# Kernel optimization log

Hardware: AMD Instinct MI355X
Metric: run time of the kernel (lower is better)

Reference implementation:

```python
import jax, jax.numpy as jnp
import numpy as np

B, T, D = 2, 2048, 1024
H = 16
HD = D // H
SCALE = 1.0 / np.sqrt(HD).astype(np.float32)


def setup_inputs() -> dict:
    key = jax.random.key(0)
    ks = jax.random.split(key, 5)
    std = 1.0 / np.sqrt(D).astype(np.float32)
    x = jax.random.normal(ks[0], (B, T, D), dtype=jnp.float32)
    Wqkvt = jax.random.normal(ks[1], (D, 4 * D), dtype=jnp.float32) * std
    bqkvt = jax.random.normal(ks[2], (4 * D,), dtype=jnp.float32) * 0.02
    Wout = jax.random.normal(ks[3], (D, D), dtype=jnp.float32) * std
    bout = jax.random.normal(ks[4], (D,), dtype=jnp.float32) * 0.02
    return {"x": x, "Wqkvt": Wqkvt, "bqkvt": bqkvt, "Wout": Wout, "bout": bout}


def reference(x, Wqkvt, bqkvt, Wout, bout):
    b, t, d = x.shape
    # fused qkvt projection -> [B,T,4,H,HD]
    qkvt = (x @ Wqkvt + bqkvt).reshape(b, t, 4, H, HD)
    # -> [B,H,T,HD] each
    q, k, v, tt = [jnp.transpose(qkvt[:, :, i], (0, 2, 1, 3)) for i in range(4)]

    # standard dot-product scores [B,H,T,T]
    scores_dot = jnp.einsum('bhqd,bhkd->bhqk', q, k)
    # triplet term: (q*t) against cumsum over keys of (k*v)/sqrt(hd)
    kv = k * v * SCALE
    kv_cum = jnp.cumsum(kv, axis=2)  # causal prefix over key positions
    scores_trip = jnp.einsum('bhqd,bhkd->bhqk', q * tt, kv_cum)

    scores = (scores_dot + scores_trip) * SCALE
    causal = jnp.triu(jnp.ones((t, t), dtype=bool), k=1)
    scores = jnp.where(causal[None, None], -jnp.inf, scores)

    attn = jax.nn.softmax(scores, axis=-1)
    out = jnp.einsum('bhqk,bhkd->bhqd', attn, v)  # [B,H,T,HD]
    out = jnp.transpose(out, (0, 2, 1, 3)).reshape(b, t, d)
    return out @ Wout + bout
```

## Files before the change

kernel.cpp:

```cpp
#include <hip/hip_runtime.h>

#define T_SEQ 2048
#define D_MODEL 1024
#define NH 16
#define HD 64
#define BH_TOT 32
#define M_ROWS 4096
#define NT 32
#define SCALE 0.125f
#define BHT (BH_TOT * T_SEQ)
#define LOG2E 1.44269504f
#define TAU 2.885f

typedef _Float16 h8 __attribute__((ext_vector_type(8)));
typedef _Float16 h4 __attribute__((ext_vector_type(4)));
typedef float f32x4 __attribute__((ext_vector_type(4)));

__device__ __forceinline__ f32x4 mfma_h(h8 a, h8 b, f32x4 c) {
    return __builtin_amdgcn_mfma_f32_16x16x32_f16(a, b, c, 0, 0, 0);
}

__device__ __forceinline__ void gload16(const _Float16* g, _Float16* l) {
    __builtin_amdgcn_global_load_lds(
        (const __attribute__((address_space(1))) unsigned int*)g,
        (__attribute__((address_space(3))) unsigned int*)l, 16, 0, 0);
}

__global__ void k_convert(const float* __restrict__ in, _Float16* __restrict__ out, int n) {
    int i = (blockIdx.x * blockDim.x + threadIdx.x) * 4;
    if (i < n) {
        float4 v = *(const float4*)(in + i);
        h4 o;
        o[0] = (_Float16)v.x; o[1] = (_Float16)v.y;
        o[2] = (_Float16)v.z; o[3] = (_Float16)v.w;
        *(h4*)(out + i) = o;
    }
}

__global__ void k_transpose(const float* __restrict__ in, _Float16* __restrict__ out, int K, int N) {
    __shared__ float tile[32][33];
    int nb = blockIdx.x * 32, kb = blockIdx.y * 32;
    int tx = threadIdx.x & 31, ty = threadIdx.x >> 5;
    #pragma unroll
    for (int i = 0; i < 32; i += 8)
        tile[ty + i][tx] = in[(size_t)(kb + ty + i) * N + (nb + tx)];
    __syncthreads();
    #pragma unroll
    for (int i = 0; i < 32; i += 8)
        out[(size_t)(nb + ty + i) * K + (kb + tx)] = (_Float16)tile[tx][ty + i];
}

template<int MODE>
__launch_bounds__(256, 2)
__global__ void k_gemm(const _Float16* __restrict__ A, const _Float16* __restrict__ Bt,
                       int M, int N, int K, const float* __restrict__ bias,
                       _Float16* __restrict__ qo, _Float16* __restrict__ kho,
                       _Float16* __restrict__ kfo, _Float16* __restrict__ vo,
                       _Float16* __restrict__ vfo, _Float16* __restrict__ to,
                       float* __restrict__ cOut)
{
    __shared__ __align__(16) _Float16 lA[2][128 * 64];
    __shared__ __align__(16) _Float16 lB[2][128 * 64];
    const int tid = threadIdx.x;
    const int wid = tid >> 6, lane = tid & 63, lrow = lane & 15, lg = lane >> 4;
    const int wm = wid >> 1, wn = wid & 1;
    const int m0 = blockIdx.x * 128, n0 = blockIdx.y * 128;

    f32x4 acc[4][4];
    #pragma unroll
    for (int i = 0; i < 4; i++)
        #pragma unroll
        for (int j = 0; j < 4; j++) acc[i][j] = (f32x4){0.f, 0.f, 0.f, 0.f};

    const int rin = lane >> 3, gcol = lane & 7;
    const int scol = (gcol ^ rin) * 8;
    const _Float16* gA = A + (size_t)(m0 + 32 * wid + rin) * K + scol;
    const _Float16* gB = Bt + (size_t)(n0 + 32 * wid + rin) * K + scol;

    const int r7 = lrow & 7;
    const int nk = K >> 6;

    #pragma unroll
    for (int i = 0; i < 4; i++) {
        gload16(gA + (size_t)(8 * i) * K, &lA[0][32 * wid * 64 + 8 * i * 64]);
        gload16(gB + (size_t)(8 * i) * K, &lB[0][32 * wid * 64 + 8 * i * 64]);
    }
    __syncthreads();

    for (int kt = 0; kt < nk; ++kt) {
        const int cur = kt & 1;
        if (kt + 1 < nk) {
            const size_t ko = (size_t)(kt + 1) * 64;
            #pragma unroll
            for (int i = 0; i < 4; i++) {
                gload16(gA + (size_t)(8 * i) * K + ko, &lA[cur ^ 1][32 * wid * 64 + 8 * i * 64]);
                gload16(gB + (size_t)(8 * i) * K + ko, &lB[cur ^ 1][32 * wid * 64 + 8 * i * 64]);
            }
        }
        h8 af[4][2], bfr[4][2];
        #pragma unroll
        for (int mi = 0; mi < 4; mi++) {
            const int row = wm * 64 + mi * 16 + lrow;
            af[mi][0] = *(const h8*)&lA[cur][row * 64 + ((lg ^ r7) * 8)];
            af[mi][1] = *(const h8*)&lA[cur][row * 64 + (((4 + lg) ^ r7) * 8)];
        }
        #pragma unroll
        for (int ni = 0; ni < 4; ni++) {
            const int row = wn * 64 + ni * 16 + lrow;
            bfr[ni][0] = *(const h8*)&lB[cur][row * 64 + ((lg ^ r7) * 8)];
            bfr[ni][1] = *(const h8*)&lB[cur][row * 64 + (((4 + lg) ^ r7) * 8)];
        }
        #pragma unroll
        for (int mi = 0; mi < 4; mi++)
            #pragma unroll
            for (int ni = 0; ni < 4; ni++) {
                acc[mi][ni] = mfma_h(af[mi][0], bfr[ni][0], acc[mi][ni]);
                acc[mi][ni] = mfma_h(af[mi][1], bfr[ni][1], acc[mi][ni]);
            }
        __syncthreads();
    }

    if (MODE == 0) {
        const int ssel = n0 >> 10;
        #pragma unroll
        for (int mi = 0; mi < 4; mi++) {
            #pragma unroll
            for (int ni = 0; ni < 4; ni++) {
                const int nn = n0 + wn * 64 + ni * 16 + lrow;
                const float bv = bias[nn];
                const int h = (nn >> 6) & 15, hd = nn & 63;
                const int mmb = m0 + wm * 64 + mi * 16 + 4 * lg;
                const int b = mmb >> 11, t0 = mmb & (T_SEQ - 1);
                const int bh = b * NH + h;
                const size_t rowb = (size_t)bh * T_SEQ;
                h4 hv;
                #pragma unroll
                for (int r = 0; r < 4; r++) hv[r] = (_Float16)(acc[mi][ni][r] + bv);
                if (ssel == 0) {
                    #pragma unroll
                    for (int r = 0; r < 4; r++) qo[(rowb + t0 + r) * HD + hd] = hv[r];
                } else if (ssel == 1) {
                    const int ksK = hd >> 5, lgK = (hd & 31) >> 3, iK = hd & 7;
                    #pragma unroll
                    for (int r = 0; r < 4; r++) {
                        const int t = t0 + r;
                        kho[(rowb + t) * HD + hd] = hv[r];
                        const int j = t >> 6, ct = (t >> 4) & 3;
                        const int laneF = (t & 15) | (lgK << 4);
                        kfo[(((size_t)bh * 32 + j) * 16 + ct * 4 + ksK) * 512 + laneF * 8 + iK] = hv[r];
                    }
                } else if (ssel == 2) {
                    #pragma unroll
                    for (int r = 0; r < 4; r++) vo[(rowb + t0 + r) * HD + hd] = hv[r];
                    const int ctV = hd >> 4, lrV = hd & 15;
                    const int j = t0 >> 6, ksV = (t0 >> 5) & 1, lgV = (t0 >> 3) & 3, i0 = t0 & 7;
                    const int laneF = lrV | (lgV << 4);
                    *(h4*)&vfo[(((size_t)bh * 32 + j) * 8 + ctV * 2 + ksV) * 512 + laneF * 8 + i0] = hv;
                } else {
                    #pragma unroll
                    for (int r = 0; r < 4; r++) to[(rowb + t0 + r) * HD + hd] = hv[r];
                }
            }
        }
    } else {
        #pragma unroll
        for (int mi = 0; mi < 4; mi++) {
            #pragma unroll
            for (int ni = 0; ni < 4; ni++) {
                const int nn = n0 + wn * 64 + ni * 16 + lrow;
                const float bv = bias[nn];
                #pragma unroll
                for (int r = 0; r < 4; r++) {
                    const int mm = m0 + wm * 64 + mi * 16 + 4 * lg + r;
                    cOut[(size_t)mm * N + nn] = acc[mi][ni][r] + bv;
                }
            }
        }
    }
}

__global__ void k_kvcum(const _Float16* __restrict__ Kh, const _Float16* __restrict__ Vh,
                        _Float16* __restrict__ KF)
{
    const int bh = blockIdx.x;
    const int w = threadIdx.x >> 6, d = threadIdx.x & 63;
    const size_t base = (size_t)bh * T_SEQ * HD + d;
    const int CH = T_SEQ / 16;
    const int t0 = w * CH;
    float s = 0.f;
    #pragma unroll 8
    for (int i = 0; i < CH; i++) {
        size_t o = base + (size_t)(t0 + i) * HD;
        s += (float)Kh[o] * (float)Vh[o];
    }
    __shared__ float tot[16][64];
    tot[w][d] = s;
    __syncthreads();
    float acc = 0.f;
    for (int ww = 0; ww < w; ww++) acc += tot[ww][d];
    const int ksK = 2 + (d >> 5), lgK = (d & 31) >> 3, iK = d & 7;
    for (int i = 0; i < CH; i++) {
        const int t = t0 + i;
        size_t o = base + (size_t)t * HD;
        acc += (float)Kh[o] * (float)Vh[o];
        const int j = t >> 6, ct = (t >> 4) & 3;
        const int laneF = (t & 15) | (lgK << 4);
        KF[(((size_t)bh * 32 + j) * 16 + ct * 4 + ksK) * 512 + laneF * 8 + iK] =
            (_Float16)(acc * SCALE);
    }
}

__launch_bounds__(256, 4)
__global__ void k_attn(const _Float16* __restrict__ Qb, const _Float16* __restrict__ Tb,
                       const _Float16* __restrict__ KF, const _Float16* __restrict__ VF,
                       _Float16* __restrict__ Op0, _Float16* __restrict__ Op1,
                       _Float16* __restrict__ Op2, _Float16* __restrict__ Op3,
                       float* __restrict__ ML, int nsplit)
{
    const int bh = blockIdx.x;
    const int pair = blockIdx.y;
    const int ksel = blockIdx.z;
    const int tid = threadIdx.x;
    const int wid = tid >> 6, lane = tid & 63, lrow = lane & 15, lg = lane >> 4;
    const _Float16* qp = Qb + (size_t)bh * T_SEQ * HD;
    const _Float16* tp = Tb + (size_t)bh * T_SEQ * HD;
    const _Float16* kfb = KF + (size_t)bh * 32 * 16 * 512;
    const _Float16* vfb = VF + (size_t)bh * 32 * 8 * 512;
    _Float16* op = (ksel == 0) ? Op0 : (ksel == 1) ? Op1 : (ksel == 2) ? Op2 : Op3;
    float* ml = ML + (size_t)ksel * BHT * 2;

    __shared__ __align__(16) _Float16 lP[4][16 * 64];

    const h8 ones = {(_Float16)1.f, (_Float16)1.f, (_Float16)1.f, (_Float16)1.f,
                     (_Float16)1.f, (_Float16)1.f, (_Float16)1.f, (_Float16)1.f};
    const float C = SCALE * LOG2E;

    for (int half = 0; half < 2; ++half) {
        const int qi = half ? (NT - 1 - pair) : pair;
        const int q0 = qi * 64;
        const int nj = qi + 1;
        const int jbeg = (nj * ksel) / nsplit;
        const int jend = (nj * (ksel + 1)) / nsplit;

        const int qrow = q0 + wid * 16 + lrow;
        h8 qf[4];
        #pragma unroll
        for (int ks = 0; ks < 2; ++ks) {
            h8 qv = *(const h8*)&qp[(size_t)qrow * HD + ks * 32 + lg * 8];
            h8 tv = *(const h8*)&tp[(size_t)qrow * HD + ks * 32 + lg * 8];
            h8 a2, b2;
            #pragma unroll
            for (int i = 0; i < 8; i++) {
                float qq = (float)qv[i] * C;
                a2[i] = (_Float16)qq;
                b2[i] = (_Float16)(qq * (float)tv[i]);
            }
            qf[ks] = a2; qf[2 + ks] = b2;
        }

        float m_r[4];
        f32x4 o[4], o4;
        #pragma unroll
        for (int r = 0; r < 4; r++) m_r[r] = -__builtin_inff();
        #pragma unroll
        for (int ct = 0; ct < 4; ct++) o[ct] = (f32x4){0.f, 0.f, 0.f, 0.f};
        o4 = (f32x4){0.f, 0.f, 0.f, 0.f};

        for (int j = jbeg; j < jend; ++j) {
            f32x4 s[4];
            #pragma unroll
            for (int ct = 0; ct < 4; ct++) {
                const _Float16* kb = kfb + ((size_t)j * 16 + ct * 4) * 512 + lane * 8;
                f32x4 sv = (f32x4){0.f, 0.f, 0.f, 0.f};
                sv = mfma_h(qf[0], *(const h8*)kb, sv);
                sv = mfma_h(qf[1], *(const h8*)(kb + 512), sv);
                sv = mfma_h(qf[2], *(const h8*)(kb + 1024), sv);
                sv = mfma_h(qf[3], *(const h8*)(kb + 1536), sv);
                s[ct] = sv;
            }
            if (j == qi) {
                #pragma unroll
                for (int ct = 0; ct < 4; ct++)
                    #pragma unroll
                    for (int r = 0; r < 4; r++) {
                        int key = j * 64 + ct * 16 + lrow;
                        int qr  = q0 + wid * 16 + 4 * lg + r;
                        if (key > qr) s[ct][r] = -__builtin_inff();
                    }
            }
            float mx[4];
            #pragma unroll
            for (int r = 0; r < 4; r++)
                mx[r] = fmaxf(fmaxf(s[0][r], s[1][r]), fmaxf(s[2][r], s[3][r]));
            bool need = (mx[0] > m_r[0] + TAU) | (mx[1] > m_r[1] + TAU) |
                        (mx[2] > m_r[2] + TAU) | (mx[3] > m_r[3] + TAU);
            if (__any(need)) {
                #pragma unroll
                for (int d = 1; d < 16; d <<= 1)
                    #pragma unroll
                    for (int r = 0; r < 4; r++) mx[r] = fmaxf(mx[r], __shfl_xor(mx[r], d, 64));
                #pragma unroll
                for (int r = 0; r < 4; r++) {
                    float mn = fmaxf(m_r[r], mx[r]);
                    float scl = __builtin_amdgcn_exp2f(m_r[r] - mn);
                    o[0][r] *= scl; o[1][r] *= scl; o[2][r] *= scl; o[3][r] *= scl;
                    o4[r] *= scl;
                    m_r[r] = mn;
                }
            }
            #pragma unroll
            for (int ct = 0; ct < 4; ct++) {
                const int col = ct * 16 + lrow;
                #pragma unroll
                for (int r = 0; r < 4; r++) {
                    float p = __builtin_amdgcn_exp2f(s[ct][r] - m_r[r]);
                    const int row = 4 * lg + r;
                    const int boff = row * 128 + ((col * 2) ^ ((row & 7) << 4) ^ ((row & 12) << 3));
                    lP[wid][boff >> 1] = (_Float16)p;
                }
            }
            h8 pa[2];
            #pragma unroll
            for (int ks = 0; ks < 2; ks++) {
                const int boff = lrow * 128 +
                    ((ks * 64 + lg * 16) ^ ((lrow & 7) << 4) ^ ((lrow & 12) << 3));
                pa[ks] = *(const h8*)((const char*)lP[wid] + boff);
            }
            o4 = mfma_h(pa[0], ones, o4);
            o4 = mfma_h(pa[1], ones, o4);
            #pragma unroll
            for (int ct = 0; ct < 4; ct++) {
                const _Float16* vb = vfb + ((size_t)j * 8 + ct * 2) * 512 + lane * 8;
                o[ct] = mfma_h(pa[0], *(const h8*)vb, o[ct]);
                o[ct] = mfma_h(pa[1], *(const h8*)(vb + 512), o[ct]);
            }
        }
        #pragma unroll
        for (int ct = 0; ct < 4; ct++)
            #pragma unroll
            for (int r = 0; r < 4; r++) {
                const int trow = q0 + wid * 16 + 4 * lg + r;
                const int d = ct * 16 + lrow;
                op[((size_t)bh * T_SEQ + trow) * HD + d] = (_Float16)o[ct][r];
            }
        if (lrow == 0) {
            #pragma unroll
            for (int r = 0; r < 4; r++) {
                const int trow = q0 + wid * 16 + 4 * lg + r;
                const size_t mi = ((size_t)bh * T_SEQ + trow) * 2;
                ml[mi] = m_r[r];
                ml[mi + 1] = o4[r];
            }
        }
    }
}

__global__ void k_combine(const _Float16* __restrict__ Op0, const _Float16* __restrict__ Op1,
                          const _Float16* __restrict__ Op2, const _Float16* __restrict__ Op3,
                          const float* __restrict__ ML, _Float16* __restrict__ AO, int nsplit)
{
    const int idx = blockIdx.x * 256 + threadIdx.x;
    const int row = idx >> 3;
    const int d0 = (idx & 7) * 8;
    const int bh = row >> 11, t = row & (T_SEQ - 1);
    const int b = bh >> 4, h = bh & 15;
    const _Float16* ops[4] = {Op0, Op1, Op2, Op3};
    float m = -__builtin_inff();
    for (int c = 0; c < nsplit; c++) m = fmaxf(m, ML[(size_t)c * BHT * 2 + 2 * row]);
    float w[4], denom = 0.f;
    for (int c = 0; c < nsplit; c++) {
        w[c] = __builtin_amdgcn_exp2f(ML[(size_t)c * BHT * 2 + 2 * row] - m);
        denom += w[c] * ML[(size_t)c * BHT * 2 + 2 * row + 1];
    }
    const float inv = 1.0f / denom;
    float accv[8];
    #pragma unroll
    for (int i = 0; i < 8; i++) accv[i] = 0.f;
    for (int c = 0; c < nsplit; c++) {
        h8 a = *(const h8*)&ops[c][(size_t)row * HD + d0];
        #pragma unroll
        for (int i = 0; i < 8; i++) accv[i] += w[c] * (float)a[i];
    }
    h8 r;
    #pragma unroll
    for (int i = 0; i < 8; i++) r[i] = (_Float16)(accv[i] * inv);
    *(h8*)&AO[((size_t)(b * T_SEQ + t)) * D_MODEL + h * HD + d0] = r;
}

extern "C" void kernel_launch(void* const* d_in, const int* in_sizes, int n_in,
                              void* d_out, int out_size, void* d_ws, size_t ws_size,
                              hipStream_t stream)
{
    const float* x     = (const float*)d_in[0];
    const float* Wqkvt = (const float*)d_in[1];
    const float* bqkvt = (const float*)d_in[2];
    const float* Wout  = (const float*)d_in[3];
    const float* bout  = (const float*)d_in[4];
    float* out = (float*)d_out;

    char* ws = (char*)d_ws;
    size_t off = 0;
    auto alloc = [&](size_t bytes) {
        char* p = ws + off;
        off += (bytes + 255) & ~(size_t)255;
        return p;
    };
    const size_t SZ = (size_t)M_ROWS * D_MODEL * 2;
    _Float16* xb  = (_Float16*)alloc(SZ);
    _Float16* wt  = (_Float16*)alloc(SZ);
    _Float16* wo  = (_Float16*)alloc((size_t)D_MODEL * D_MODEL * 2);
    _Float16* Qh  = (_Float16*)alloc(SZ);
    _Float16* Kh  = (_Float16*)alloc(SZ);
    _Float16* Vh  = (_Float16*)alloc(SZ);
    _Float16* Th  = (_Float16*)alloc(SZ);
    _Float16* KF  = (_Float16*)alloc(SZ * 2);
    _Float16* VF  = (_Float16*)alloc(SZ);
    _Float16* AO  = (_Float16*)alloc(SZ);
    _Float16* Op3 = (_Float16*)alloc(SZ);
    const size_t need4 = off;

    const int nsplit = (ws_size >= need4) ? 4 : 2;

    _Float16* Op0 = xb;
    _Float16* Op1 = Vh;
    _Float16* Op2 = Kh;
    float*    ML  = (float*)wt;

    k_convert<<<4096, 256, 0, stream>>>(x, xb, M_ROWS * D_MODEL);
    k_transpose<<<dim3(128, 32), 256, 0, stream>>>(Wqkvt, wt, D_MODEL, 4 * D_MODEL);
    k_transpose<<<dim3(32, 32), 256, 0, stream>>>(Wout, wo, D_MODEL, D_MODEL);
    k_gemm<0><<<dim3(32, 32), 256, 0, stream>>>(xb, wt, M_ROWS, 4 * D_MODEL, D_MODEL,
                                                bqkvt, Qh, Kh, KF, Vh, VF, Th, nullptr);
    k_kvcum<<<BH_TOT, 1024, 0, stream>>>(Kh, Vh, KF);
    k_attn<<<dim3(BH_TOT, NT / 2, nsplit), 256, 0, stream>>>(Qh, Th, KF, VF,
                                                             Op0, Op1, Op2, Op3, ML, nsplit);
    k_combine<<<BHT * HD / 8 / 256, 256, 0, stream>>>(Op0, Op1, Op2, Op3, ML, AO, nsplit);
    k_gemm<1><<<dim3(32, 8), 256, 0, stream>>>(AO, wo, M_ROWS, D_MODEL, D_MODEL,
                                               bout, nullptr, nullptr, nullptr, nullptr,
                                               nullptr, nullptr, out);
}
```

Baseline: 188.2 us.

## Stage K/V tiles through double-buffered LDS with half-width key steps in attention

```diff
diff --git a/kernel.cpp b/kernel.cpp
--- a/kernel.cpp
+++ b/kernel.cpp
@@ -229,11 +229,23 @@
     _Float16* op = (ksel == 0) ? Op0 : (ksel == 1) ? Op1 : (ksel == 2) ? Op2 : Op3;
     float* ml = ML + (size_t)ksel * BHT * 2;
 
-    __shared__ __align__(16) _Float16 lP[4][16 * 64];
+    __shared__ __align__(16) _Float16 ldsK[2][8 * 512];
+    __shared__ __align__(16) _Float16 ldsV[2][4 * 512];
+    __shared__ __align__(16) _Float16 lP[4][16 * 32];
 
     const h8 ones = {(_Float16)1.f, (_Float16)1.f, (_Float16)1.f, (_Float16)1.f,
                      (_Float16)1.f, (_Float16)1.f, (_Float16)1.f, (_Float16)1.f};
     const float C = SCALE * LOG2E;
+
+    auto stage = [&](int st, int buf) {
+        const _Float16* kfj = kfb + ((size_t)(st >> 1) * 16 + (st & 1) * 8) * 512;
+        #pragma unroll
+        for (int i = 0; i < 2; i++)
+            gload16(kfj + i * 2048 + wid * 512 + lane * 8,
+                    &ldsK[buf][i * 2048 + wid * 512]);
+        const _Float16* vfj = vfb + ((size_t)(st >> 1) * 8 + wid * 2 + (st & 1)) * 512;
+        gload16(vfj + lane * 8, &ldsV[buf][wid * 512]);
+    };
 
     for (int half = 0; half < 2; ++half) {
         const int qi = half ? (NT - 1 - pair) : pair;
@@ -241,6 +253,7 @@
         const int nj = qi + 1;
         const int jbeg = (nj * ksel) / nsplit;
         const int jend = (nj * (ksel + 1)) / nsplit;
+        const int sbeg = 2 * jbeg, send = 2 * jend;
 
         const int qrow = q0 + wid * 16 + lrow;
         h8 qf[4];
@@ -266,32 +279,37 @@
         for (int ct = 0; ct < 4; ct++) o[ct] = (f32x4){0.f, 0.f, 0.f, 0.f};
         o4 = (f32x4){0.f, 0.f, 0.f, 0.f};
 
-        for (int j = jbeg; j < jend; ++j) {
-            f32x4 s[4];
-            #pragma unroll
-            for (int ct = 0; ct < 4; ct++) {
-                const _Float16* kb = kfb + ((size_t)j * 16 + ct * 4) * 512 + lane * 8;
+        if (sbeg < send) stage(sbeg, 0);
+        __syncthreads();
+
+        int cur = 0;
+        for (int st = sbeg; st < send; ++st) {
+            if (st + 1 < send) stage(st + 1, cur ^ 1);
+
+            f32x4 s[2];
+            #pragma unroll
+            for (int c2 = 0; c2 < 2; c2++) {
+                const _Float16* kb = &ldsK[cur][(c2 * 4) * 512] + lane * 8;
                 f32x4 sv = (f32x4){0.f, 0.f, 0.f, 0.f};
                 sv = mfma_h(qf[0], *(const h8*)kb, sv);
                 sv = mfma_h(qf[1], *(const h8*)(kb + 512), sv);
                 sv = mfma_h(qf[2], *(const h8*)(kb + 1024), sv);
                 sv = mfma_h(qf[3], *(const h8*)(kb + 1536), sv);
-                s[ct] = sv;
-            }
-            if (j == qi) {
-                #pragma unroll
-                for (int ct = 0; ct < 4; ct++)
+                s[c2] = sv;
+            }
+            if ((st >> 1) == qi) {
+                #pragma unroll
+                for (int c2 = 0; c2 < 2; c2++)
                     #pragma unroll
                     for (int r = 0; r < 4; r++) {
-                        int key = j * 64 + ct * 16 + lrow;
+                        int key = (st >> 1) * 64 + (st & 1) * 32 + c2 * 16 + lrow;
                         int qr  = q0 + wid * 16 + 4 * lg + r;
-                        if (key > qr) s[ct][r] = -__builtin_inff();
+                        if (key > qr) s[c2][r] = -__builtin_inff();
                     }
             }
             float mx[4];
             #pragma unroll
-            for (int r = 0; r < 4; r++)
-                mx[r] = fmaxf(fmaxf(s[0][r], s[1][r]), fmaxf(s[2][r], s[3][r]));
+            for (int r = 0; r < 4; r++) mx[r] = fmaxf(s[0][r], s[1][r]);
             bool need = (mx[0] > m_r[0] + TAU) | (mx[1] > m_r[1] + TAU) |
                         (mx[2] > m_r[2] + TAU) | (mx[3] > m_r[3] + TAU);
             if (__any(need)) {
@@ -309,31 +327,29 @@
                 }
             }
             #pragma unroll
-            for (int ct = 0; ct < 4; ct++) {
-                const int col = ct * 16 + lrow;
+            for (int c2 = 0; c2 < 2; c2++) {
+                const int col = c2 * 16 + lrow;
                 #pragma unroll
                 for (int r = 0; r < 4; r++) {
-                    float p = __builtin_amdgcn_exp2f(s[ct][r] - m_r[r]);
+                    float p = __builtin_amdgcn_exp2f(s[c2][r] - m_r[r]);
                     const int row = 4 * lg + r;
-                    const int boff = row * 128 + ((col * 2) ^ ((row & 7) << 4) ^ ((row & 12) << 3));
+                    const int boff = row * 64 + ((col * 2) ^ ((row >> 2) << 4));
                     lP[wid][boff >> 1] = (_Float16)p;
                 }
             }
-            h8 pa[2];
-            #pragma unroll
-            for (int ks = 0; ks < 2; ks++) {
-                const int boff = lrow * 128 +
-                    ((ks * 64 + lg * 16) ^ ((lrow & 7) << 4) ^ ((lrow & 12) << 3));
-                pa[ks] = *(const h8*)((const char*)lP[wid] + boff);
-            }
-            o4 = mfma_h(pa[0], ones, o4);
-            o4 = mfma_h(pa[1], ones, o4);
+            h8 pa;
+            {
+                const int boff = lrow * 64 + ((lg * 16) ^ ((lrow >> 2) << 4));
+                pa = *(const h8*)((const char*)lP[wid] + boff);
+            }
+            o4 = mfma_h(pa, ones, o4);
             #pragma unroll
             for (int ct = 0; ct < 4; ct++) {
-                const _Float16* vb = vfb + ((size_t)j * 8 + ct * 2) * 512 + lane * 8;
-                o[ct] = mfma_h(pa[0], *(const h8*)vb, o[ct]);
-                o[ct] = mfma_h(pa[1], *(const h8*)(vb + 512), o[ct]);
-            }
+                const _Float16* vb = &ldsV[cur][ct * 512] + lane * 8;
+                o[ct] = mfma_h(pa, *(const h8*)vb, o[ct]);
+            }
+            __syncthreads();
+            cur ^= 1;
         }
         #pragma unroll
         for (int ct = 0; ct < 4; ct++)
@@ -417,9 +433,8 @@
     _Float16* VF  = (_Float16*)alloc(SZ);
     _Float16* AO  = (_Float16*)alloc(SZ);
     _Float16* Op3 = (_Float16*)alloc(SZ);
-    const size_t need4 = off;
-
-    const int nsplit = (ws_size >= need4) ? 4 : 2;
+
+    const int nsplit = 2;
 
     _Float16* Op0 = xb;
     _Float16* Op1 = Vh;
```

New measurement: 178.6 us. 5.1% less time.
